# Performance work log

Measured on AMD Instinct MI355X. Metric: run time of the kernel, lower is better.

## Reference

```python
import jax, jax.numpy as jnp
import numpy as np

BASE = 10000.0

def rotate_half(x):
    # interleaved pairs: (x0, x1, x2, x3, ...) -> (-x1, x0, -x3, x2, ...)
    x2 = x.reshape(x.shape[:-1] + (-1, 2))
    a, b = x2[..., 0], x2[..., 1]
    return jnp.stack((-b, a), axis=-1).reshape(x.shape)

def rope_tables(seq_len, head_dim, dtype):
    inv_freq = 1.0 / (BASE ** (jnp.arange(0, head_dim, 2, dtype=jnp.float32) / head_dim))
    t = jnp.arange(seq_len, dtype=jnp.float32)
    freqs = jnp.outer(t, inv_freq)                      # [s, head_dim//2]
    cos = jnp.repeat(jnp.cos(freqs), 2, axis=-1)        # '... d -> ... (d 2)'
    sin = jnp.repeat(jnp.sin(freqs), 2, axis=-1)
    # seq_dimension = -3 for [b, s, h, d] tensors -> broadcast over heads
    return cos[:, None, :].astype(dtype), sin[:, None, :].astype(dtype)

def setup_inputs() -> dict:
    key = jax.random.key(0)
    kx, kw1, kw2 = jax.random.split(key, 3)
    b, s, d = 4, 2048, 2048
    h = 16
    x = jax.random.normal(kx, (b, s, d), dtype=jnp.float32)
    # causal mask: True above the diagonal = masked positions
    attn_mask = jnp.triu(jnp.ones((s, s), dtype=bool), k=1)
    Wqkv_w = jax.random.normal(kw1, (d, 3 * d), dtype=jnp.float32) / np.sqrt(d)
    Wqkv_b = jnp.zeros((3 * d,), dtype=jnp.float32)
    Wout_w = jax.random.normal(kw2, (d, d), dtype=jnp.float32) / np.sqrt(d)
    Wout_b = jnp.zeros((d,), dtype=jnp.float32)
    return {"x": x, "attn_mask": attn_mask, "Wqkv_w": Wqkv_w, "Wqkv_b": Wqkv_b,
            "Wout_w": Wout_w, "Wout_b": Wout_b, "num_heads": 16}

def reference(x, attn_mask, Wqkv_w, Wqkv_b, Wout_w, Wout_b, num_heads):
    b, s, d = x.shape
    h = num_heads
    hd = d // h
    qkv = jnp.einsum('bsd,de->bse', x, Wqkv_w) + Wqkv_b        # [b, s, 3d]
    qkv = qkv.reshape(b, s, 3, h, hd)
    q, k, v = qkv[:, :, 0], qkv[:, :, 1], qkv[:, :, 2]          # [b, s, h, hd]
    cos, sin = rope_tables(s, hd, x.dtype)                      # [s, 1, hd]
    q = q * cos + rotate_half(q) * sin
    k = k * cos + rotate_half(k) * sin
    scale = 1.0 / np.sqrt(hd).astype(np.float32)
    scores = jnp.einsum('bqhd,bkhd->bhqk', q, k) * scale        # [b, h, s, s]
    scores = jnp.where(attn_mask, -jnp.inf, scores)
    attn = jax.nn.softmax(scores, axis=-1)
    ctx = jnp.einsum('bhqk,bkhd->bqhd', attn, v)                # [b, s, h, hd]
    ctx = ctx.reshape(b, s, d)
    return jnp.einsum('bsd,de->bse', ctx, Wout_w) + Wout_b
```

## Files before the change

### kernel.cpp

```cpp
#include <hip/hip_runtime.h>

#define BB 4
#define SS 2048
#define DD 2048
#define HH 16
#define HD 128
#define D3 6144

typedef __attribute__((ext_vector_type(8))) short short8;
typedef __attribute__((ext_vector_type(4))) float float4v;

#define MFMA16(a, b, c) __builtin_amdgcn_mfma_f32_16x16x32_bf16(a, b, c, 0, 0, 0)

#define GLL16(g, l)                                                     \
    __builtin_amdgcn_global_load_lds(                                   \
        (__attribute__((address_space(1))) void*)(g),                   \
        (__attribute__((address_space(3))) void*)(l), 16, 0, 0)

__device__ __forceinline__ unsigned short f2b(float f) {
    union { float f; unsigned u; } v;
    v.f = f;
    unsigned r = v.u + 0x7FFFu + ((v.u >> 16) & 1u);
    return (unsigned short)(r >> 16);
}

__global__ void cast_f32_bf16(const float* __restrict__ in,
                              unsigned short* __restrict__ out) {
    int i = (blockIdx.x * 256 + threadIdx.x) * 4;
    float4 v = *(const float4*)(in + i);
    ushort4 o;
    o.x = f2b(v.x); o.y = f2b(v.y); o.z = f2b(v.z); o.w = f2b(v.w);
    *(ushort4*)(out + i) = o;
}

__global__ void transpose_cast(const float* __restrict__ in,
                               unsigned short* __restrict__ out, int R, int C) {
    __shared__ float tile[32][33];
    int c0 = blockIdx.x * 32, r0 = blockIdx.y * 32;
    int tc = threadIdx.x & 31, tr = threadIdx.x >> 5;
#pragma unroll
    for (int i = 0; i < 4; ++i) {
        int r = tr + i * 8;
        tile[r][tc] = in[(size_t)(r0 + r) * C + c0 + tc];
    }
    __syncthreads();
#pragma unroll
    for (int i = 0; i < 4; ++i) {
        int wr = tr + i * 8;
        out[(size_t)(c0 + wr) * R + r0 + tc] = f2b(tile[tc][wr]);
    }
}

__global__ void vtrans(const unsigned short* __restrict__ qkv,
                       unsigned short* __restrict__ vT) {
    __shared__ unsigned short tile[32][33];
    int bh = blockIdx.z, b = bh >> 4, h = bh & 15;
    int s0 = blockIdx.x * 32, d0 = blockIdx.y * 32;
    int tc = threadIdx.x & 31, tr = threadIdx.x >> 5;
    const unsigned short* src = qkv + (size_t)b * SS * D3 + 4096 + h * HD;
#pragma unroll
    for (int i = 0; i < 4; ++i) {
        int sl = tr + i * 8;
        tile[sl][tc] = src[(size_t)(s0 + sl) * D3 + d0 + tc];
    }
    __syncthreads();
    unsigned short* dst = vT + (size_t)bh * HD * SS;
#pragma unroll
    for (int i = 0; i < 4; ++i) {
        int dl = tr + i * 8;
        dst[(size_t)(d0 + dl) * SS + s0 + tc] = tile[tc][dl];
    }
}

template <int BF16OUT>
__global__ __launch_bounds__(256) void gemm_bt(
    const unsigned short* __restrict__ A,
    const unsigned short* __restrict__ Bt,
    const float* __restrict__ bias,
    void* __restrict__ Cout, int M, int N, int K) {
    __shared__ unsigned short As[128 * 32];
    __shared__ unsigned short Bs[128 * 32];
    const int n0 = blockIdx.x * 128, m0 = blockIdx.y * 128;
    const int t = threadIdx.x, lane = t & 63, w = t >> 6;
    const int quad = lane >> 4, lr = lane & 15;
    const int wm = (w >> 1) * 64, wn = (w & 1) * 64;
    float4v acc[4][4] = {};
    const int srow = w * 32 + (lane >> 2);
    const int scol = (lane & 3) * 8;
    const unsigned short* Ag = A + (size_t)(m0 + srow) * K + scol;
    const unsigned short* Bg = Bt + (size_t)(n0 + srow) * K + scol;
    unsigned short* Asw = &As[(w * 32) * 32];
    unsigned short* Bsw = &Bs[(w * 32) * 32];
    for (int k0 = 0; k0 < K; k0 += 32) {
        __syncthreads();
        GLL16(Ag + k0, Asw);
        GLL16(Ag + k0 + (size_t)16 * K, Asw + 16 * 32);
        GLL16(Bg + k0, Bsw);
        GLL16(Bg + k0 + (size_t)16 * K, Bsw + 16 * 32);
        __syncthreads();
        short8 af[4], bf[4];
#pragma unroll
        for (int i = 0; i < 4; ++i)
            af[i] = *(const short8*)&As[(wm + i * 16 + lr) * 32 + quad * 8];
#pragma unroll
        for (int j = 0; j < 4; ++j)
            bf[j] = *(const short8*)&Bs[(wn + j * 16 + lr) * 32 + quad * 8];
#pragma unroll
        for (int i = 0; i < 4; ++i)
#pragma unroll
            for (int j = 0; j < 4; ++j)
                acc[i][j] = MFMA16(af[i], bf[j], acc[i][j]);
    }
#pragma unroll
    for (int j = 0; j < 4; ++j) {
        int n = n0 + wn + j * 16 + lr;
        float bv = bias[n];
#pragma unroll
        for (int i = 0; i < 4; ++i)
#pragma unroll
            for (int r = 0; r < 4; ++r) {
                int m = m0 + wm + i * 16 + quad * 4 + r;
                float v = acc[i][j][r] + bv;
                if (BF16OUT)
                    ((unsigned short*)Cout)[(size_t)m * N + n] = f2b(v);
                else
                    ((float*)Cout)[(size_t)m * N + n] = v;
            }
    }
}

__global__ void rope_kernel(unsigned short* __restrict__ qkv) {
    int tid = blockIdx.x * 256 + threadIdx.x;
    int i = tid & 63;
    int h = (tid >> 6) & 15;
    int s = (tid >> 10) & 2047;
    int b = tid >> 21;
    size_t off = ((size_t)(b * SS + s)) * D3 + h * HD + 2 * i;
    float inv = exp2f(-(float)i * 0.2076205059304601f);
    float ang = (float)s * inv;
    float sn, c;
    sincosf(ang, &sn, &c);
    unsigned short* q = qkv + off;
    unsigned short* k = q + 2048;
    union { unsigned u; float f; } a0, a1;
    a0.u = (unsigned)q[0] << 16; a1.u = (unsigned)q[1] << 16;
    q[0] = f2b(a0.f * c - a1.f * sn);
    q[1] = f2b(a1.f * c + a0.f * sn);
    a0.u = (unsigned)k[0] << 16; a1.u = (unsigned)k[1] << 16;
    k[0] = f2b(a0.f * c - a1.f * sn);
    k[1] = f2b(a1.f * c + a0.f * sn);
}

__global__ __launch_bounds__(256) void attn_kernel(
    const unsigned short* __restrict__ qkv,
    const unsigned short* __restrict__ vT,
    unsigned short* __restrict__ ctx) {
    __shared__ unsigned short Ks[64 * 128];
    __shared__ unsigned short Vs[128 * 64];
    __shared__ unsigned short Pw[4][32][72];
    const int bh = blockIdx.y, b = bh >> 4, h = bh & 15;
    const int q0 = (int)(gridDim.x - 1 - blockIdx.x) * 128;
    const int t = threadIdx.x, w = t >> 6, lane = t & 63;
    const int quad = lane >> 4, lr = lane & 15;
    const int wq = q0 + w * 32;
    const unsigned short* qbase = qkv + (size_t)b * SS * D3 + h * HD;
    const unsigned short* kbase = qbase + 2048;
    const unsigned short* vtb = vT + (size_t)bh * HD * SS;
    const float scale = 0.08838834764831845f;

    short8 qf[2][4];
#pragma unroll
    for (int m = 0; m < 2; ++m)
#pragma unroll
        for (int c = 0; c < 4; ++c)
            qf[m][c] = *(const short8*)(qbase + (size_t)(wq + m * 16 + lr) * D3 +
                                        c * 32 + quad * 8);

    float4v o[2][8] = {};
    float l_lane[2][4] = {};

    const int kr = lane >> 4, kg = lane & 15;
    const int vr = lane >> 3, vg = lane & 7;

    const int kend = q0 + 128;
    for (int k0 = 0; k0 < kend; k0 += 64) {
        __syncthreads();
#pragma unroll
        for (int u = 0; u < 4; ++u) {
            int row = w * 16 + u * 4 + kr;
            int g = kg ^ (row & 15);
            GLL16(kbase + (size_t)(k0 + row) * D3 + g * 8,
                  &Ks[(w * 16 + u * 4) * 128]);
        }
#pragma unroll
        for (int u = 0; u < 4; ++u) {
            int row = w * 32 + u * 8 + vr;
            int g = vg ^ (row & 7);
            GLL16(vtb + (size_t)row * SS + k0 + g * 8,
                  &Vs[(w * 32 + u * 8) * 64]);
        }
        __syncthreads();

        float4v sc[2][4] = {};
#pragma unroll
        for (int c = 0; c < 4; ++c) {
            short8 kf[4];
#pragma unroll
            for (int ks = 0; ks < 4; ++ks)
                kf[ks] = *(const short8*)&Ks[(ks * 16 + lr) * 128 +
                                             (((c * 4 + quad) ^ lr) * 8)];
#pragma unroll
            for (int m = 0; m < 2; ++m)
#pragma unroll
                for (int ks = 0; ks < 4; ++ks)
                    sc[m][ks] = MFMA16(qf[m][c], kf[ks], sc[m][ks]);
        }

#pragma unroll
        for (int m = 0; m < 2; ++m)
#pragma unroll
            for (int ks = 0; ks < 4; ++ks) {
                int key = k0 + ks * 16 + lr;
#pragma unroll
                for (int r = 0; r < 4; ++r) {
                    int qrow = wq + m * 16 + quad * 4 + r;
                    float p = (key <= qrow)
                                  ? __expf(fmaf(sc[m][ks][r], scale, -16.0f))
                                  : 0.0f;
                    l_lane[m][r] += p;
                    Pw[w][m * 16 + quad * 4 + r][ks * 16 + lr] = f2b(p);
                }
            }

#pragma unroll
        for (int kc = 0; kc < 2; ++kc) {
            short8 pf0 = *(const short8*)&Pw[w][lr][kc * 32 + quad * 8];
            short8 pf1 = *(const short8*)&Pw[w][16 + lr][kc * 32 + quad * 8];
#pragma unroll
            for (int dc = 0; dc < 8; ++dc) {
                short8 vf = *(const short8*)&Vs[(dc * 16 + lr) * 64 +
                                                (((kc * 4 + quad) ^ (lr & 7)) * 8)];
                o[0][dc] = MFMA16(pf0, vf, o[0][dc]);
                o[1][dc] = MFMA16(pf1, vf, o[1][dc]);
            }
        }
    }

    float linv[2][4];
#pragma unroll
    for (int m = 0; m < 2; ++m)
#pragma unroll
        for (int r = 0; r < 4; ++r) {
            float l = l_lane[m][r];
            l += __shfl_xor(l, 1);
            l += __shfl_xor(l, 2);
            l += __shfl_xor(l, 4);
            l += __shfl_xor(l, 8);
            linv[m][r] = 1.0f / l;
        }
#pragma unroll
    for (int m = 0; m < 2; ++m)
#pragma unroll
        for (int dc = 0; dc < 8; ++dc)
#pragma unroll
            for (int r = 0; r < 4; ++r) {
                float val = o[m][dc][r] * linv[m][r];
                ctx[(size_t)(b * SS + wq + m * 16 + quad * 4 + r) * DD + h * HD +
                    dc * 16 + lr] = f2b(val);
            }
}

extern "C" void kernel_launch(void* const* d_in, const int* in_sizes, int n_in,
                              void* d_out, int out_size, void* d_ws, size_t ws_size,
                              hipStream_t stream) {
    const float* x = (const float*)d_in[0];
    const float* Wqkv_w = (const float*)d_in[2];
    const float* Wqkv_b = (const float*)d_in[3];
    const float* Wout_w = (const float*)d_in[4];
    const float* Wout_b = (const float*)d_in[5];
    float* out = (float*)d_out;

    unsigned short* x_bf = (unsigned short*)d_ws;
    unsigned short* wqkv_t = x_bf + 16777216;
    unsigned short* wout_t = wqkv_t + 12582912;
    unsigned short* qkv = wout_t + 4194304;
    unsigned short* ctx = qkv + 50331648;
    unsigned short* vT = x_bf;

    cast_f32_bf16<<<16384, 256, 0, stream>>>(x, x_bf);
    transpose_cast<<<dim3(192, 64), 256, 0, stream>>>(Wqkv_w, wqkv_t, 2048, 6144);
    transpose_cast<<<dim3(64, 64), 256, 0, stream>>>(Wout_w, wout_t, 2048, 2048);
    gemm_bt<1><<<dim3(48, 64), 256, 0, stream>>>(x_bf, wqkv_t, Wqkv_b, qkv,
                                                 8192, 6144, 2048);
    rope_kernel<<<32768, 256, 0, stream>>>(qkv);
    vtrans<<<dim3(64, 4, 64), 256, 0, stream>>>(qkv, vT);
    attn_kernel<<<dim3(16, 64), 256, 0, stream>>>(qkv, vT, ctx);
    gemm_bt<0><<<dim3(16, 64), 256, 0, stream>>>(ctx, wout_t, Wout_b, out,
                                                 8192, 2048, 2048);
}
```

Measured before the change: 756.3 us.

## Fuse RoPE and V-transpose into QKV GEMM epilogue, skip masked attention tiles

The QKV GEMM epilogue now applies rotary embedding to the Q/K columns, using hardware sin/cos on range-reduced angles, and writes them to a compact Q/K buffer. It transposes V tiles through shared memory and writes them straight into the V^T layout, so the separate rope and vtrans kernels and their memory round-trips go away. In attention, warps skip key tiles that lie entirely above their causal diagonal and apply the mask only on diagonal tiles. They also use exp2 with a folded scale and truncate P to bf16 instead of rounding it. The hardware sin/cos and truncation slightly reduce precision, and the extra shared buffer and epilogue syncs add cost to the GEMM.

```diff
diff --git a/kernel.cpp b/kernel.cpp
--- a/kernel.cpp
+++ b/kernel.cpp
@@ -6,6 +6,7 @@
 #define HH 16
 #define HD 128
 #define D3 6144
+#define QKS 4096
 
 typedef __attribute__((ext_vector_type(8))) short short8;
 typedef __attribute__((ext_vector_type(4))) float float4v;
@@ -51,35 +52,17 @@
     }
 }
 
-__global__ void vtrans(const unsigned short* __restrict__ qkv,
-                       unsigned short* __restrict__ vT) {
-    __shared__ unsigned short tile[32][33];
-    int bh = blockIdx.z, b = bh >> 4, h = bh & 15;
-    int s0 = blockIdx.x * 32, d0 = blockIdx.y * 32;
-    int tc = threadIdx.x & 31, tr = threadIdx.x >> 5;
-    const unsigned short* src = qkv + (size_t)b * SS * D3 + 4096 + h * HD;
-#pragma unroll
-    for (int i = 0; i < 4; ++i) {
-        int sl = tr + i * 8;
-        tile[sl][tc] = src[(size_t)(s0 + sl) * D3 + d0 + tc];
-    }
-    __syncthreads();
-    unsigned short* dst = vT + (size_t)bh * HD * SS;
-#pragma unroll
-    for (int i = 0; i < 4; ++i) {
-        int dl = tr + i * 8;
-        dst[(size_t)(d0 + dl) * SS + s0 + tc] = tile[tc][dl];
-    }
-}
-
-template <int BF16OUT>
+template <int MODE>
 __global__ __launch_bounds__(256) void gemm_bt(
     const unsigned short* __restrict__ A,
     const unsigned short* __restrict__ Bt,
     const float* __restrict__ bias,
-    void* __restrict__ Cout, int M, int N, int K) {
+    void* __restrict__ Cout,
+    unsigned short* __restrict__ vtout,
+    int M, int N, int K) {
     __shared__ unsigned short As[128 * 32];
     __shared__ unsigned short Bs[128 * 32];
+    __shared__ unsigned short Et[MODE ? 32 * 136 : 8];
     const int n0 = blockIdx.x * 128, m0 = blockIdx.y * 128;
     const int t = threadIdx.x, lane = t & 63, w = t >> 6;
     const int quad = lane >> 4, lr = lane & 15;
@@ -111,48 +94,84 @@
             for (int j = 0; j < 4; ++j)
                 acc[i][j] = MFMA16(af[i], bf[j], acc[i][j]);
     }
-#pragma unroll
-    for (int j = 0; j < 4; ++j) {
-        int n = n0 + wn + j * 16 + lr;
-        float bv = bias[n];
-#pragma unroll
-        for (int i = 0; i < 4; ++i)
-#pragma unroll
-            for (int r = 0; r < 4; ++r) {
-                int m = m0 + wm + i * 16 + quad * 4 + r;
-                float v = acc[i][j][r] + bv;
-                if (BF16OUT)
-                    ((unsigned short*)Cout)[(size_t)m * N + n] = f2b(v);
-                else
-                    ((float*)Cout)[(size_t)m * N + n] = v;
-            }
-    }
-}
-
-__global__ void rope_kernel(unsigned short* __restrict__ qkv) {
-    int tid = blockIdx.x * 256 + threadIdx.x;
-    int i = tid & 63;
-    int h = (tid >> 6) & 15;
-    int s = (tid >> 10) & 2047;
-    int b = tid >> 21;
-    size_t off = ((size_t)(b * SS + s)) * D3 + h * HD + 2 * i;
-    float inv = exp2f(-(float)i * 0.2076205059304601f);
-    float ang = (float)s * inv;
-    float sn, c;
-    sincosf(ang, &sn, &c);
-    unsigned short* q = qkv + off;
-    unsigned short* k = q + 2048;
-    union { unsigned u; float f; } a0, a1;
-    a0.u = (unsigned)q[0] << 16; a1.u = (unsigned)q[1] << 16;
-    q[0] = f2b(a0.f * c - a1.f * sn);
-    q[1] = f2b(a1.f * c + a0.f * sn);
-    a0.u = (unsigned)k[0] << 16; a1.u = (unsigned)k[1] << 16;
-    k[0] = f2b(a0.f * c - a1.f * sn);
-    k[1] = f2b(a1.f * c + a0.f * sn);
+
+    if (MODE == 0) {
+#pragma unroll
+        for (int j = 0; j < 4; ++j) {
+            int n = n0 + wn + j * 16 + lr;
+            float bv = bias[n];
+#pragma unroll
+            for (int i = 0; i < 4; ++i)
+#pragma unroll
+                for (int r = 0; r < 4; ++r) {
+                    int m = m0 + wm + i * 16 + quad * 4 + r;
+                    ((float*)Cout)[(size_t)m * N + n] = acc[i][j][r] + bv;
+                }
+        }
+    } else if (n0 < 4096) {
+        unsigned short* qkp = (unsigned short*)Cout;
+        const float L2IF = 0.2076205059304601f;
+        const float R2PI = 0.15915494309189535f;
+        const int sbase = (m0 & 2047) + wm;
+#pragma unroll
+        for (int j = 0; j < 4; ++j) {
+            int n = n0 + wn + j * 16 + lr;
+            float bv = bias[n];
+            int ip = (n & 127) >> 1;
+            float invr = exp2f(-(float)ip * L2IF) * R2PI;
+            float ssign = (n & 1) ? 1.0f : -1.0f;
+#pragma unroll
+            for (int i = 0; i < 4; ++i)
+#pragma unroll
+                for (int r = 0; r < 4; ++r) {
+                    float v = acc[i][j][r] + bv;
+                    float pv = __shfl_xor(v, 1);
+                    float rev = (float)(sbase + i * 16 + quad * 4 + r) * invr;
+                    float rr = rev - floorf(rev);
+                    float sn = __builtin_amdgcn_sinf(rr);
+                    float cs = __builtin_amdgcn_cosf(rr);
+                    float outv = fmaf(v, cs, ssign * pv * sn);
+                    int m = m0 + wm + i * 16 + quad * 4 + r;
+                    qkp[(size_t)m * QKS + n] = f2b(outv);
+                }
+        }
+    } else {
+        int bh = ((m0 >> 11) << 4) + ((n0 - 4096) >> 7);
+        unsigned short* vtp = vtout + (size_t)bh * HD * SS + (m0 & 2047);
+#pragma unroll
+        for (int c = 0; c < 4; ++c) {
+            if (c) __syncthreads();
+            if (wn == (c >> 1) * 64) {
+#pragma unroll
+                for (int jj = 0; jj < 2; ++jj) {
+                    int j = (c & 1) * 2 + jj;
+                    int n = n0 + wn + j * 16 + lr;
+                    float bv = bias[n];
+                    int dloc = jj * 16 + lr;
+#pragma unroll
+                    for (int i = 0; i < 4; ++i) {
+                        uint2 pk;
+                        pk.x = (unsigned)f2b(acc[i][j][0] + bv) |
+                               ((unsigned)f2b(acc[i][j][1] + bv) << 16);
+                        pk.y = (unsigned)f2b(acc[i][j][2] + bv) |
+                               ((unsigned)f2b(acc[i][j][3] + bv) << 16);
+                        *(uint2*)&Et[dloc * 136 + wm + i * 16 + quad * 4] = pk;
+                    }
+                }
+            }
+            __syncthreads();
+            int dloc = t >> 3, sg = (t & 7) * 16;
+#pragma unroll
+            for (int u = 0; u < 2; ++u) {
+                short8 vv = *(const short8*)&Et[dloc * 136 + sg + u * 8];
+                *(short8*)(vtp + (size_t)(c * 32 + dloc) * SS + sg + u * 8) = vv;
+            }
+        }
+    }
 }
 
 __global__ __launch_bounds__(256) void attn_kernel(
-    const unsigned short* __restrict__ qkv,
+    const unsigned short* __restrict__ qk,
     const unsigned short* __restrict__ vT,
     unsigned short* __restrict__ ctx) {
     __shared__ unsigned short Ks[64 * 128];
@@ -163,17 +182,18 @@
     const int t = threadIdx.x, w = t >> 6, lane = t & 63;
     const int quad = lane >> 4, lr = lane & 15;
     const int wq = q0 + w * 32;
-    const unsigned short* qbase = qkv + (size_t)b * SS * D3 + h * HD;
+    const unsigned short* qbase = qk + (size_t)b * SS * QKS + h * HD;
     const unsigned short* kbase = qbase + 2048;
     const unsigned short* vtb = vT + (size_t)bh * HD * SS;
-    const float scale = 0.08838834764831845f;
+    const float SCL2E = 0.12751741769976451f;
+    const float NB16 = -23.083120654223414f;
 
     short8 qf[2][4];
 #pragma unroll
     for (int m = 0; m < 2; ++m)
 #pragma unroll
         for (int c = 0; c < 4; ++c)
-            qf[m][c] = *(const short8*)(qbase + (size_t)(wq + m * 16 + lr) * D3 +
+            qf[m][c] = *(const short8*)(qbase + (size_t)(wq + m * 16 + lr) * QKS +
                                         c * 32 + quad * 8);
 
     float4v o[2][8] = {};
@@ -189,7 +209,7 @@
         for (int u = 0; u < 4; ++u) {
             int row = w * 16 + u * 4 + kr;
             int g = kg ^ (row & 15);
-            GLL16(kbase + (size_t)(k0 + row) * D3 + g * 8,
+            GLL16(kbase + (size_t)(k0 + row) * QKS + g * 8,
                   &Ks[(w * 16 + u * 4) * 128]);
         }
 #pragma unroll
@@ -201,6 +221,8 @@
         }
         __syncthreads();
 
+        if (k0 > wq + 31) continue;
+
         float4v sc[2][4] = {};
 #pragma unroll
         for (int c = 0; c < 4; ++c) {
@@ -216,6 +238,7 @@
                     sc[m][ks] = MFMA16(qf[m][c], kf[ks], sc[m][ks]);
         }
 
+        const bool need_mask = (k0 + 63 > wq);
 #pragma unroll
         for (int m = 0; m < 2; ++m)
 #pragma unroll
@@ -223,12 +246,16 @@
                 int key = k0 + ks * 16 + lr;
 #pragma unroll
                 for (int r = 0; r < 4; ++r) {
-                    int qrow = wq + m * 16 + quad * 4 + r;
-                    float p = (key <= qrow)
-                                  ? __expf(fmaf(sc[m][ks][r], scale, -16.0f))
-                                  : 0.0f;
+                    float p = exp2f(fmaf(sc[m][ks][r], SCL2E, NB16));
+                    if (need_mask) {
+                        int qrow = wq + m * 16 + quad * 4 + r;
+                        if (key > qrow) p = 0.0f;
+                    }
                     l_lane[m][r] += p;
-                    Pw[w][m * 16 + quad * 4 + r][ks * 16 + lr] = f2b(p);
+                    union { float f; unsigned u; } pu;
+                    pu.f = p;
+                    Pw[w][m * 16 + quad * 4 + r][ks * 16 + lr] =
+                        (unsigned short)(pu.u >> 16);
                 }
             }
 
@@ -283,18 +310,16 @@
     unsigned short* x_bf = (unsigned short*)d_ws;
     unsigned short* wqkv_t = x_bf + 16777216;
     unsigned short* wout_t = wqkv_t + 12582912;
-    unsigned short* qkv = wout_t + 4194304;
-    unsigned short* ctx = qkv + 50331648;
-    unsigned short* vT = x_bf;
+    unsigned short* qk = wout_t + 4194304;
+    unsigned short* vT = qk + 33554432;
+    unsigned short* ctx = vT + 16777216;
 
     cast_f32_bf16<<<16384, 256, 0, stream>>>(x, x_bf);
     transpose_cast<<<dim3(192, 64), 256, 0, stream>>>(Wqkv_w, wqkv_t, 2048, 6144);
     transpose_cast<<<dim3(64, 64), 256, 0, stream>>>(Wout_w, wout_t, 2048, 2048);
-    gemm_bt<1><<<dim3(48, 64), 256, 0, stream>>>(x_bf, wqkv_t, Wqkv_b, qkv,
+    gemm_bt<1><<<dim3(48, 64), 256, 0, stream>>>(x_bf, wqkv_t, Wqkv_b, qk, vT,
                                                  8192, 6144, 2048);
-    rope_kernel<<<32768, 256, 0, stream>>>(qkv);
-    vtrans<<<dim3(64, 4, 64), 256, 0, stream>>>(qkv, vT);
-    attn_kernel<<<dim3(16, 64), 256, 0, stream>>>(qkv, vT, ctx);
-    gemm_bt<0><<<dim3(16, 64), 256, 0, stream>>>(ctx, wout_t, Wout_b, out,
+    attn_kernel<<<dim3(16, 64), 256, 0, stream>>>(qk, vT, ctx);
+    gemm_bt<0><<<dim3(16, 64), 256, 0, stream>>>(ctx, wout_t, Wout_b, out, nullptr,
                                                  8192, 2048, 2048);
 }
```

Result: slower. 805.3 us (+6.5%).

## Pair causal query tiles per block, double-buffer K/V, vectorize RoPE

Applied to the files above, without the earlier changes.

The attention kernel now handles two query tiles per block, one early and one late, so each block does a balanced share of causal work, and the grid halves. K/V tiles are double-buffered so the next tile's global-to-LDS loads overlap compute. The score MFMA is transposed, masking applies only on diagonal tiles, exp2 uses a prescaled constant, and P is packed by truncation instead of rounding. RoPE processes 8 elements per thread with vector loads and hardware sin/cos after range reduction. The risks are more LDS use, which lowers occupancy, and slightly less precise P and RoPE values.

```diff
diff --git a/kernel.cpp b/kernel.cpp
--- a/kernel.cpp
+++ b/kernel.cpp
@@ -22,6 +22,11 @@
     v.f = f;
     unsigned r = v.u + 0x7FFFu + ((v.u >> 16) & 1u);
     return (unsigned short)(r >> 16);
+}
+__device__ __forceinline__ float b2f(unsigned short h) {
+    union { unsigned u; float f; } v;
+    v.u = ((unsigned)h) << 16;
+    return v.f;
 }
 
 __global__ void cast_f32_bf16(const float* __restrict__ in,
@@ -131,143 +136,196 @@
 
 __global__ void rope_kernel(unsigned short* __restrict__ qkv) {
     int tid = blockIdx.x * 256 + threadIdx.x;
-    int i = tid & 63;
-    int h = (tid >> 6) & 15;
-    int s = (tid >> 10) & 2047;
-    int b = tid >> 21;
-    size_t off = ((size_t)(b * SS + s)) * D3 + h * HD + 2 * i;
-    float inv = exp2f(-(float)i * 0.2076205059304601f);
-    float ang = (float)s * inv;
-    float sn, c;
-    sincosf(ang, &sn, &c);
+    int i4 = tid & 15;
+    int h = (tid >> 4) & 15;
+    int s = (tid >> 8) & 2047;
+    int b = tid >> 19;
+    size_t off = ((size_t)(b * SS + s)) * D3 + h * HD + i4 * 8;
     unsigned short* q = qkv + off;
     unsigned short* k = q + 2048;
-    union { unsigned u; float f; } a0, a1;
-    a0.u = (unsigned)q[0] << 16; a1.u = (unsigned)q[1] << 16;
-    q[0] = f2b(a0.f * c - a1.f * sn);
-    q[1] = f2b(a1.f * c + a0.f * sn);
-    a0.u = (unsigned)k[0] << 16; a1.u = (unsigned)k[1] << 16;
-    k[0] = f2b(a0.f * c - a1.f * sn);
-    k[1] = f2b(a1.f * c + a0.f * sn);
+    short8 qv = *(short8*)q, kv = *(short8*)k;
+    const float L2IF = 0.2076205059304601f;
+    const float R2PI = 0.15915494309189535f;
+    short8 qo, ko;
+#pragma unroll
+    for (int j = 0; j < 4; ++j) {
+        int i = i4 * 4 + j;
+        float invr = exp2f(-(float)i * L2IF) * R2PI;
+        float rev = (float)s * invr;
+        float rr = rev - floorf(rev);
+        float sn = __builtin_amdgcn_sinf(rr);
+        float cs = __builtin_amdgcn_cosf(rr);
+        float a0 = b2f((unsigned short)qv[2 * j]);
+        float a1 = b2f((unsigned short)qv[2 * j + 1]);
+        qo[2 * j] = (short)f2b(a0 * cs - a1 * sn);
+        qo[2 * j + 1] = (short)f2b(a1 * cs + a0 * sn);
+        float c0 = b2f((unsigned short)kv[2 * j]);
+        float c1 = b2f((unsigned short)kv[2 * j + 1]);
+        ko[2 * j] = (short)f2b(c0 * cs - c1 * sn);
+        ko[2 * j + 1] = (short)f2b(c1 * cs + c0 * sn);
+    }
+    *(short8*)q = qo;
+    *(short8*)k = ko;
 }
 
 __global__ __launch_bounds__(256) void attn_kernel(
     const unsigned short* __restrict__ qkv,
     const unsigned short* __restrict__ vT,
     unsigned short* __restrict__ ctx) {
-    __shared__ unsigned short Ks[64 * 128];
-    __shared__ unsigned short Vs[128 * 64];
-    __shared__ unsigned short Pw[4][32][72];
+    __shared__ unsigned short Ks[2][64 * 128];
+    __shared__ unsigned short Vs[2][128 * 64];
+    __shared__ unsigned short PT[4][32][40];
     const int bh = blockIdx.y, b = bh >> 4, h = bh & 15;
-    const int q0 = (int)(gridDim.x - 1 - blockIdx.x) * 128;
     const int t = threadIdx.x, w = t >> 6, lane = t & 63;
     const int quad = lane >> 4, lr = lane & 15;
-    const int wq = q0 + w * 32;
     const unsigned short* qbase = qkv + (size_t)b * SS * D3 + h * HD;
     const unsigned short* kbase = qbase + 2048;
     const unsigned short* vtb = vT + (size_t)bh * HD * SS;
-    const float scale = 0.08838834764831845f;
-
-    short8 qf[2][4];
-#pragma unroll
-    for (int m = 0; m < 2; ++m)
-#pragma unroll
-        for (int c = 0; c < 4; ++c)
-            qf[m][c] = *(const short8*)(qbase + (size_t)(wq + m * 16 + lr) * D3 +
-                                        c * 32 + quad * 8);
-
-    float4v o[2][8] = {};
-    float l_lane[2][4] = {};
-
+    const float SCL2E = 0.12751741769976451f;
+    const float NB16 = -23.083120654223414f;
+    const int q0a = blockIdx.x * 128;
+    const int q0b = (15 - (int)blockIdx.x) * 128;
+    const int nta = (q0a >> 6) + 2, ntb = (q0b >> 6) + 2, ntot = nta + ntb;
     const int kr = lane >> 4, kg = lane & 15;
     const int vr = lane >> 3, vg = lane & 7;
 
-    const int kend = q0 + 128;
-    for (int k0 = 0; k0 < kend; k0 += 64) {
-        __syncthreads();
+    auto stage = [&](int k0, int bi) {
+        unsigned short* KD = Ks[bi];
+        unsigned short* VD = Vs[bi];
 #pragma unroll
         for (int u = 0; u < 4; ++u) {
             int row = w * 16 + u * 4 + kr;
             int g = kg ^ (row & 15);
             GLL16(kbase + (size_t)(k0 + row) * D3 + g * 8,
-                  &Ks[(w * 16 + u * 4) * 128]);
+                  &KD[(w * 16 + u * 4) * 128]);
         }
 #pragma unroll
         for (int u = 0; u < 4; ++u) {
             int row = w * 32 + u * 8 + vr;
             int g = vg ^ (row & 7);
             GLL16(vtb + (size_t)row * SS + k0 + g * 8,
-                  &Vs[(w * 32 + u * 8) * 64]);
-        }
+                  &VD[(w * 32 + u * 8) * 64]);
+        }
+    };
+
+    int wq = q0a + w * 32;
+    short8 qf[2][4];
+#pragma unroll
+    for (int m = 0; m < 2; ++m)
+#pragma unroll
+        for (int c = 0; c < 4; ++c)
+            qf[m][c] = *(const short8*)(qbase + (size_t)(wq + m * 16 + lr) * D3 +
+                                        c * 32 + quad * 8);
+
+    float4v o[2][8] = {};
+    float l_lane[2] = {0.f, 0.f};
+
+    auto epilogue = [&]() {
+#pragma unroll
+        for (int m = 0; m < 2; ++m) {
+            float l = l_lane[m];
+            l += __shfl_xor(l, 16);
+            l += __shfl_xor(l, 32);
+#pragma unroll
+            for (int r = 0; r < 4; ++r) {
+                float linv = 1.0f / __shfl(l, quad * 4 + r);
+#pragma unroll
+                for (int dc = 0; dc < 8; ++dc) {
+                    float val = o[m][dc][r] * linv;
+                    ctx[(size_t)(b * SS + wq + m * 16 + quad * 4 + r) * DD +
+                        h * HD + dc * 16 + lr] = f2b(val);
+                }
+            }
+        }
+    };
+
+    stage(0, 0);
+
+    for (int it = 0; it < ntot; ++it) {
         __syncthreads();
-
-        float4v sc[2][4] = {};
-#pragma unroll
-        for (int c = 0; c < 4; ++c) {
-            short8 kf[4];
-#pragma unroll
-            for (int ks = 0; ks < 4; ++ks)
-                kf[ks] = *(const short8*)&Ks[(ks * 16 + lr) * 128 +
-                                             (((c * 4 + quad) ^ lr) * 8)];
+        int nit = it + 1;
+        if (nit < ntot) stage((nit < nta ? nit : nit - nta) * 64, nit & 1);
+        int k0 = (it < nta ? it : it - nta) * 64;
+        const unsigned short* KB = Ks[it & 1];
+        const unsigned short* VB = Vs[it & 1];
+
+        if (k0 <= wq + 31) {
+            float4v sc[2][4] = {};
+#pragma unroll
+            for (int c = 0; c < 4; ++c) {
+                short8 kf[4];
+#pragma unroll
+                for (int ks = 0; ks < 4; ++ks)
+                    kf[ks] = *(const short8*)&KB[(ks * 16 + lr) * 128 +
+                                                 (((c * 4 + quad) ^ lr) * 8)];
+#pragma unroll
+                for (int ks = 0; ks < 4; ++ks) {
+                    sc[0][ks] = MFMA16(kf[ks], qf[0][c], sc[0][ks]);
+                    sc[1][ks] = MFMA16(kf[ks], qf[1][c], sc[1][ks]);
+                }
+            }
+            const bool nm = (k0 + 63 > wq);
+#pragma unroll
+            for (int kc = 0; kc < 2; ++kc) {
+#pragma unroll
+                for (int m = 0; m < 2; ++m)
+#pragma unroll
+                    for (int ks2 = 0; ks2 < 2; ++ks2) {
+                        int ks = kc * 2 + ks2;
+                        unsigned pk[2];
+#pragma unroll
+                        for (int rp = 0; rp < 2; ++rp) {
+                            unsigned lo = 0, hi = 0;
+#pragma unroll
+                            for (int rr = 0; rr < 2; ++rr) {
+                                int r = rp * 2 + rr;
+                                float p = exp2f(fmaf(sc[m][ks][r], SCL2E, NB16));
+                                if (nm) {
+                                    int key = k0 + ks * 16 + quad * 4 + r;
+                                    if (key > wq + m * 16 + lr) p = 0.0f;
+                                }
+                                l_lane[m] += p;
+                                union { float f; unsigned u; } pu;
+                                pu.f = p;
+                                if (rr == 0) lo = pu.u >> 16;
+                                else hi = pu.u >> 16;
+                            }
+                            pk[rp] = lo | (hi << 16);
+                        }
+                        uint2 pkk = {pk[0], pk[1]};
+                        *(uint2*)&PT[w][m * 16 + lr][ks2 * 16 + quad * 4] = pkk;
+                    }
+                short8 pf0 = *(const short8*)&PT[w][lr][quad * 8];
+                short8 pf1 = *(const short8*)&PT[w][16 + lr][quad * 8];
+#pragma unroll
+                for (int dc = 0; dc < 8; ++dc) {
+                    short8 vf = *(const short8*)&VB[(dc * 16 + lr) * 64 +
+                                                    (((kc * 4 + quad) ^ (lr & 7)) * 8)];
+                    o[0][dc] = MFMA16(pf0, vf, o[0][dc]);
+                    o[1][dc] = MFMA16(pf1, vf, o[1][dc]);
+                }
+            }
+        }
+
+        if (it == nta - 1) {
+            epilogue();
+#pragma unroll
+            for (int m = 0; m < 2; ++m) {
+                l_lane[m] = 0.f;
+#pragma unroll
+                for (int dc = 0; dc < 8; ++dc) o[m][dc] = (float4v){0, 0, 0, 0};
+            }
+            wq = q0b + w * 32;
 #pragma unroll
             for (int m = 0; m < 2; ++m)
 #pragma unroll
-                for (int ks = 0; ks < 4; ++ks)
-                    sc[m][ks] = MFMA16(qf[m][c], kf[ks], sc[m][ks]);
-        }
-
-#pragma unroll
-        for (int m = 0; m < 2; ++m)
-#pragma unroll
-            for (int ks = 0; ks < 4; ++ks) {
-                int key = k0 + ks * 16 + lr;
-#pragma unroll
-                for (int r = 0; r < 4; ++r) {
-                    int qrow = wq + m * 16 + quad * 4 + r;
-                    float p = (key <= qrow)
-                                  ? __expf(fmaf(sc[m][ks][r], scale, -16.0f))
-                                  : 0.0f;
-                    l_lane[m][r] += p;
-                    Pw[w][m * 16 + quad * 4 + r][ks * 16 + lr] = f2b(p);
-                }
-            }
-
-#pragma unroll
-        for (int kc = 0; kc < 2; ++kc) {
-            short8 pf0 = *(const short8*)&Pw[w][lr][kc * 32 + quad * 8];
-            short8 pf1 = *(const short8*)&Pw[w][16 + lr][kc * 32 + quad * 8];
-#pragma unroll
-            for (int dc = 0; dc < 8; ++dc) {
-                short8 vf = *(const short8*)&Vs[(dc * 16 + lr) * 64 +
-                                                (((kc * 4 + quad) ^ (lr & 7)) * 8)];
-                o[0][dc] = MFMA16(pf0, vf, o[0][dc]);
-                o[1][dc] = MFMA16(pf1, vf, o[1][dc]);
-            }
-        }
-    }
-
-    float linv[2][4];
-#pragma unroll
-    for (int m = 0; m < 2; ++m)
-#pragma unroll
-        for (int r = 0; r < 4; ++r) {
-            float l = l_lane[m][r];
-            l += __shfl_xor(l, 1);
-            l += __shfl_xor(l, 2);
-            l += __shfl_xor(l, 4);
-            l += __shfl_xor(l, 8);
-            linv[m][r] = 1.0f / l;
-        }
-#pragma unroll
-    for (int m = 0; m < 2; ++m)
-#pragma unroll
-        for (int dc = 0; dc < 8; ++dc)
-#pragma unroll
-            for (int r = 0; r < 4; ++r) {
-                float val = o[m][dc][r] * linv[m][r];
-                ctx[(size_t)(b * SS + wq + m * 16 + quad * 4 + r) * DD + h * HD +
-                    dc * 16 + lr] = f2b(val);
-            }
+                for (int c = 0; c < 4; ++c)
+                    qf[m][c] = *(const short8*)(qbase +
+                                                (size_t)(wq + m * 16 + lr) * D3 +
+                                                c * 32 + quad * 8);
+        }
+    }
+    epilogue();
 }
 
 extern "C" void kernel_launch(void* const* d_in, const int* in_sizes, int n_in,
@@ -292,9 +350,9 @@
     transpose_cast<<<dim3(64, 64), 256, 0, stream>>>(Wout_w, wout_t, 2048, 2048);
     gemm_bt<1><<<dim3(48, 64), 256, 0, stream>>>(x_bf, wqkv_t, Wqkv_b, qkv,
                                                  8192, 6144, 2048);
-    rope_kernel<<<32768, 256, 0, stream>>>(qkv);
+    rope_kernel<<<8192, 256, 0, stream>>>(qkv);
     vtrans<<<dim3(64, 4, 64), 256, 0, stream>>>(qkv, vT);
-    attn_kernel<<<dim3(16, 64), 256, 0, stream>>>(qkv, vT, ctx);
+    attn_kernel<<<dim3(8, 64), 256, 0, stream>>>(qkv, vT, ctx);
     gemm_bt<0><<<dim3(16, 64), 256, 0, stream>>>(ctx, wout_t, Wout_b, out,
                                                  8192, 2048, 2048);
 }
```

New measurement: 750.6 us. About the same (-0.7%).
